# Performance work log

Measured on AMD Instinct MI355X. Metric: run time of the kernel, lower is better.

The kernel has to match this reference:

```python
import jax, jax.numpy as jnp
import numpy as np

N = 50000        # nodes
E = 800000       # edges (avg degree 16)
F_IN = 128
H = 128
C = 16


def setup_inputs() -> dict:
    key = jax.random.key(0)
    ks = jax.random.split(key, 12)
    x = jax.random.normal(ks[0], (N, F_IN), dtype=jnp.float32)
    edges = jax.random.randint(ks[1], (2, E), 0, N, dtype=jnp.int32)
    dims = [(F_IN, H), (H, H // 2), (H // 2, H // 4), (H // 4, H // 8), (H // 8, C)]
    params = {}
    for i, (di, do) in enumerate(dims):
        params[f"W{i+1}"] = jax.random.normal(ks[2 + 2 * i], (di, do), dtype=jnp.float32) * (1.0 / np.sqrt(di)).astype(np.float32)
        params[f"b{i+1}"] = jax.random.normal(ks[3 + 2 * i], (do,), dtype=jnp.float32) * 0.01
    return {"x": x, "edges": edges, **params}


def reference(x, edges, W1, b1, W2, b2, W3, b3, W4, b4, W5, b5):
    src, dst = edges[0], edges[1]
    ones = jnp.ones((E,), x.dtype)
    # symmetric ('both') normalization with degree clamped to >= 1 (DGL GraphConv default)
    out_deg = jnp.clip(jax.ops.segment_sum(ones, src, num_segments=N), 1.0, None)
    in_deg = jnp.clip(jax.ops.segment_sum(ones, dst, num_segments=N), 1.0, None)
    norm_src = (out_deg ** -0.5)[:, None]   # [N,1]
    norm_dst = (in_deg ** -0.5)[:, None]    # [N,1]

    def graph_conv(h, W, b):
        h = h @ W                                  # dense transform first (out <= in)
        msgs = (h * norm_src)[src]                 # [E, d_out] gather
        agg = jax.ops.segment_sum(msgs, dst, num_segments=N)  # scatter-add SpMM
        return agg * norm_dst + b

    h = x
    for W, b in ((W1, b1), (W2, b2), (W3, b3), (W4, b4), (W5, b5)):
        h = jax.nn.relu(graph_conv(h, W, b))
    return h
```

## Files before the change

### kernel.cpp

```cpp
#include <hip/hip_runtime.h>
#include <hip/hip_bf16.h>


#define THREADS 256
#define HIST_B 256
#define HWORDS 12500

typedef __attribute__((ext_vector_type(8))) short short8_t;
typedef __attribute__((ext_vector_type(4))) float float4_t;

__device__ __forceinline__ unsigned short f2bf_rne(float f) {
    unsigned u = __builtin_bit_cast(unsigned, f);
    unsigned r = u + 0x7fffu + ((u >> 16) & 1u);
    return (unsigned short)(r >> 16);
}
__device__ __forceinline__ float bf2f(unsigned short h) {
    return __builtin_bit_cast(float, ((unsigned)h) << 16);
}

__global__ __launch_bounds__(THREADS)
void hist_kernel(const int* __restrict__ src, const int* __restrict__ dst,
                 unsigned* __restrict__ p_src, unsigned* __restrict__ p_dst,
                 unsigned char* __restrict__ rank, int E, int chunk) {
    __shared__ unsigned bins[HWORDS];
    const bool is_dst = blockIdx.x < HIST_B;
    const int b = is_dst ? blockIdx.x : blockIdx.x - HIST_B;
    const int t = threadIdx.x;
    const int e0 = b * chunk;
    int e1 = e0 + chunk; if (e1 > E) e1 = E;
    const int* __restrict__ idx = is_dst ? dst : src;
    unsigned* __restrict__ pout = is_dst ? p_dst : p_src;

    for (int w = t; w < HWORDS; w += THREADS) bins[w] = 0;
    __syncthreads();
    for (int e = e0 + t; e < e1; e += THREADS) {
        int d = idx[e];
        unsigned sh = (unsigned)(d & 3) * 8u;
        unsigned old = atomicAdd(&bins[d >> 2], 1u << sh);
        if (is_dst) rank[e] = (unsigned char)((old >> sh) & 0xffu);
    }
    __syncthreads();
    for (int w = t; w < HWORDS; w += THREADS)
        pout[(size_t)b * HWORDS + w] = bins[w];
}

__global__ __launch_bounds__(THREADS)
void reduce_scanA_kernel(const unsigned* __restrict__ p_src, unsigned* __restrict__ p_dst,
                         int* __restrict__ deg_dst,
                         float* __restrict__ norm_src, float* __restrict__ norm_dst,
                         int* __restrict__ partials, int N) {
    __shared__ int red[THREADS];
    const int t = threadIdx.x;
    const int w = blockIdx.x * THREADS + t;
    int degsum = 0;
    if (w < HWORDS) {
        unsigned s = 0;
#pragma unroll 4
        for (int b = 0; b < HIST_B; ++b) s += p_src[(size_t)b * HWORDS + w];

        unsigned run = 0;
#pragma unroll 4
        for (int b = 0; b < HIST_B; ++b) {
            size_t i = (size_t)b * HWORDS + w;
            unsigned v = p_dst[i];
            p_dst[i] = run;
            run += v;
        }

#pragma unroll
        for (int l = 0; l < 4; ++l) {
            int node = 4 * w + l;
            int dd = (int)((run >> (8 * l)) & 0xffu);
            int ds = (int)((s   >> (8 * l)) & 0xffu);
            deg_dst[node] = dd;
            norm_dst[node] = rsqrtf((float)(dd < 1 ? 1 : dd));
            norm_src[node] = rsqrtf((float)(ds < 1 ? 1 : ds));
            degsum += dd;
        }
    }
    red[t] = degsum;
    __syncthreads();
#pragma unroll
    for (int off = THREADS / 2; off > 0; off >>= 1) {
        if (t < off) red[t] += red[t + off];
        __syncthreads();
    }
    if (t == 0) partials[blockIdx.x] = red[0];
}

__global__ __launch_bounds__(THREADS)
void scanB_kernel(int* __restrict__ partials, int* __restrict__ row_ptr,
                  int nb, int N) {
    __shared__ int s[THREADS];
    int t = threadIdx.x;
    int v = (t < nb) ? partials[t] : 0;
    s[t] = v;
    __syncthreads();
#pragma unroll
    for (int off = 1; off < THREADS; off <<= 1) {
        int u = 0;
        if (t >= off) u = s[t - off];
        __syncthreads();
        s[t] += u;
        __syncthreads();
    }
    if (t < nb) partials[t] = s[t] - v;
    if (t == THREADS - 1) row_ptr[N] = s[t];
}

__global__ __launch_bounds__(THREADS)
void scanC_kernel(const int* __restrict__ deg_dst, const int* __restrict__ partials,
                  int* __restrict__ row_ptr, int N) {
    __shared__ int s[THREADS];
    const int t = threadIdx.x;
    const int base = blockIdx.x * 1024 + t * 4;
    int d0 = 0, d1 = 0, d2 = 0, d3 = 0;
    if (base + 3 < N) {
        int4 d = *(const int4*)&deg_dst[base];
        d0 = d.x; d1 = d.y; d2 = d.z; d3 = d.w;
    } else {
        if (base + 0 < N) d0 = deg_dst[base + 0];
        if (base + 1 < N) d1 = deg_dst[base + 1];
        if (base + 2 < N) d2 = deg_dst[base + 2];
        if (base + 3 < N) d3 = deg_dst[base + 3];
    }
    int tsum = d0 + d1 + d2 + d3;
    s[t] = tsum;
    __syncthreads();
#pragma unroll
    for (int off = 1; off < THREADS; off <<= 1) {
        int u = 0;
        if (t >= off) u = s[t - off];
        __syncthreads();
        s[t] += u;
        __syncthreads();
    }
    int pre = partials[blockIdx.x] + s[t] - tsum;
    if (base + 0 < N) row_ptr[base + 0] = pre; pre += d0;
    if (base + 1 < N) row_ptr[base + 1] = pre; pre += d1;
    if (base + 2 < N) row_ptr[base + 2] = pre; pre += d2;
    if (base + 3 < N) row_ptr[base + 3] = pre;
}

__global__ __launch_bounds__(THREADS)
void scatter_kernel(const int* __restrict__ src, const int* __restrict__ dst,
                    const unsigned char* __restrict__ rank,
                    const int* __restrict__ row_ptr, const unsigned* __restrict__ p_dst,
                    int* __restrict__ col, int E, int chunk) {
    const int b = blockIdx.x;
    const int e0 = b * chunk;
    int e1 = e0 + chunk; if (e1 > E) e1 = E;
    for (int e = e0 + threadIdx.x; e < e1; e += THREADS) {
        int d = dst[e];
        unsigned sh = (unsigned)(d & 3) * 8u;
        unsigned pre = (p_dst[(size_t)b * HWORDS + (d >> 2)] >> sh) & 0xffu;
        col[row_ptr[d] + (int)pre + (int)rank[e]] = src[e];
    }
}

__device__ __forceinline__ void conv_one(const float* __restrict__ W, short* __restrict__ hi,
                                         short* __restrict__ lo, int K, int NOUT, int STR, int i) {
    int n = i / STR;
    int kk = i % STR;
    float v = (kk < K) ? W[(size_t)kk * NOUT + n] : 0.f;
    unsigned short h = f2bf_rne(v);
    hi[i] = (short)h;
    lo[i] = (short)f2bf_rne(v - bf2f(h));
}

__global__ __launch_bounds__(THREADS)
void convert_all_kernel(const float* W1, const float* W2, const float* W3,
                        const float* W4, const float* W5,
                        short* w1h, short* w1l, short* w2h, short* w2l,
                        short* w3h, short* w3l, short* w4h, short* w4l,
                        short* w5h, short* w5l) {
    int i = blockIdx.x * blockDim.x + threadIdx.x;
    if      (i < 17408)                    conv_one(W1, w1h, w1l, 128, 128, 136, i);
    else if ((i -= 17408) < 8704)          conv_one(W2, w2h, w2l, 128, 64, 136, i);
    else if ((i -= 8704) < 2304)           conv_one(W3, w3h, w3l, 64, 32, 72, i);
    else if ((i -= 2304) < 640)            conv_one(W4, w4h, w4l, 32, 16, 40, i);
    else if ((i -= 640) < 640)             conv_one(W5, w5h, w5l, 16, 16, 40, i);
}

template<int K, int NOUT>
__global__ __launch_bounds__(THREADS)
void gemm_mfma_kernel(const float* __restrict__ A, const short* __restrict__ wt_hi,
                      const short* __restrict__ wt_lo, const float* __restrict__ norm,
                      short* __restrict__ outq, float* __restrict__ qscale, int M) {
    constexpr int Kp  = (K + 31) & ~31;
    constexpr int STR = Kp + 8;
    constexpr int NT  = NOUT / 16;

    __shared__ short lh[NOUT * STR];
    __shared__ short ll[NOUT * STR];

    const int tid = threadIdx.x;
    {
        constexpr int CNT = NOUT * STR / 2;
        const int* gh = (const int*)wt_hi;
        const int* gl = (const int*)wt_lo;
        int* sh = (int*)lh;
        int* sl = (int*)ll;
        for (int i = tid; i < CNT; i += THREADS) { sh[i] = gh[i]; sl[i] = gl[i]; }
    }
    __syncthreads();

    const int w    = tid >> 6;
    const int lane = tid & 63;
    const int ln   = lane & 15;
    const int quad = lane >> 4;
    const int row  = blockIdx.x * 64 + w * 16 + ln;
    const bool rv  = row < M;

    float4_t acc[NT];
#pragma unroll
    for (int i = 0; i < NT; ++i) acc[i] = (float4_t){0.f, 0.f, 0.f, 0.f};

#pragma unroll
    for (int kt = 0; kt < Kp / 32; ++kt) {
        const int k0 = kt * 32 + quad * 8;
        float a[8];
        if (rv && k0 < K) {
            float4 v0 = *(const float4*)&A[(size_t)row * K + k0];
            float4 v1 = *(const float4*)&A[(size_t)row * K + k0 + 4];
            a[0] = v0.x; a[1] = v0.y; a[2] = v0.z; a[3] = v0.w;
            a[4] = v1.x; a[5] = v1.y; a[6] = v1.z; a[7] = v1.w;
        } else {
#pragma unroll
            for (int j = 0; j < 8; ++j) a[j] = 0.f;
        }
        short8_t ahi, alo;
#pragma unroll
        for (int j = 0; j < 8; ++j) {
            unsigned short h = f2bf_rne(a[j]);
            ahi[j] = (short)h;
            alo[j] = (short)f2bf_rne(a[j] - bf2f(h));
        }
#pragma unroll
        for (int nt = 0; nt < NT; ++nt) {
            const int bidx = (nt * 16 + ln) * STR + kt * 32 + quad * 8;
            short8_t bh = *(const short8_t*)&lh[bidx];
            short8_t bl = *(const short8_t*)&ll[bidx];
            acc[nt] = __builtin_amdgcn_mfma_f32_16x16x32_bf16(ahi, bh, acc[nt], 0, 0, 0);
            acc[nt] = __builtin_amdgcn_mfma_f32_16x16x32_bf16(ahi, bl, acc[nt], 0, 0, 0);
            acc[nt] = __builtin_amdgcn_mfma_f32_16x16x32_bf16(alo, bh, acc[nt], 0, 0, 0);
        }
    }

    const int orow = blockIdx.x * 64 + w * 16 + quad * 4;
#pragma unroll
    for (int i = 0; i < 4; ++i) {
        int r = orow + i;
        float m = 0.f;
#pragma unroll
        for (int nt = 0; nt < NT; ++nt) m = fmaxf(m, fabsf(acc[nt][i]));
#pragma unroll
        for (int off = 1; off < 16; off <<= 1) m = fmaxf(m, __shfl_xor(m, off));
        float s = (r < M) ? norm[r] : 0.f;
        float rowmax = m * s;
        float inv = (rowmax > 0.f) ? (32767.f / rowmax) : 0.f;
        if (r < M) {
            if (ln == 0) qscale[r] = rowmax * (1.f / 32767.f);
#pragma unroll
            for (int nt = 0; nt < NT; ++nt)
                outq[(size_t)r * NOUT + nt * 16 + ln] =
                    (short)(int)__builtin_rintf(acc[nt][i] * s * inv);
        }
    }
}

template<int D>
__global__ __launch_bounds__(THREADS)
void agg_q_kernel(const short* __restrict__ tq, const float* __restrict__ qscale,
                  const int* __restrict__ row_ptr, const int* __restrict__ col,
                  const float* __restrict__ norm_dst, const float* __restrict__ bias,
                  float* __restrict__ out, int N) {
    constexpr int TPN = D / 8;
    constexpr int NPB = THREADS / TPN;
    const int tid  = threadIdx.x;
    const int ln   = tid % TPN;
    const int g    = tid / TPN;
    const int node = blockIdx.x * NPB + g;
    if (node >= N) return;

    const int beg = row_ptr[node];
    const int end = row_ptr[node + 1];

    float acc[8];
#pragma unroll
    for (int c = 0; c < 8; ++c) acc[c] = 0.f;

    int j = beg;
    for (; j + 3 < end; j += 4) {
        int s0 = col[j], s1 = col[j + 1], s2 = col[j + 2], s3 = col[j + 3];
        short8_t v0 = *(const short8_t*)&tq[(size_t)s0 * D + ln * 8];
        short8_t v1 = *(const short8_t*)&tq[(size_t)s1 * D + ln * 8];
        short8_t v2 = *(const short8_t*)&tq[(size_t)s2 * D + ln * 8];
        short8_t v3 = *(const short8_t*)&tq[(size_t)s3 * D + ln * 8];
        float c0 = qscale[s0], c1 = qscale[s1], c2 = qscale[s2], c3 = qscale[s3];
#pragma unroll
        for (int c = 0; c < 8; ++c)
            acc[c] += (float)v0[c] * c0 + (float)v1[c] * c1
                    + (float)v2[c] * c2 + (float)v3[c] * c3;
    }
    for (; j < end; ++j) {
        int s0 = col[j];
        short8_t v0 = *(const short8_t*)&tq[(size_t)s0 * D + ln * 8];
        float c0 = qscale[s0];
#pragma unroll
        for (int c = 0; c < 8; ++c) acc[c] += (float)v0[c] * c0;
    }

    float nd = norm_dst[node];
    float4 b0 = *(const float4*)&bias[ln * 8];
    float4 b1 = *(const float4*)&bias[ln * 8 + 4];
    float4 o0, o1;
    o0.x = fmaxf(acc[0] * nd + b0.x, 0.f);
    o0.y = fmaxf(acc[1] * nd + b0.y, 0.f);
    o0.z = fmaxf(acc[2] * nd + b0.z, 0.f);
    o0.w = fmaxf(acc[3] * nd + b0.w, 0.f);
    o1.x = fmaxf(acc[4] * nd + b1.x, 0.f);
    o1.y = fmaxf(acc[5] * nd + b1.y, 0.f);
    o1.z = fmaxf(acc[6] * nd + b1.z, 0.f);
    o1.w = fmaxf(acc[7] * nd + b1.w, 0.f);
    *(float4*)&out[(size_t)node * D + ln * 8] = o0;
    *(float4*)&out[(size_t)node * D + ln * 8 + 4] = o1;
}

extern "C" void kernel_launch(void* const* d_in, const int* in_sizes, int n_in,
                              void* d_out, int out_size, void* d_ws, size_t ws_size,
                              hipStream_t stream) {
    const float* x     = (const float*)d_in[0];
    const int*   edges = (const int*)d_in[1];
    const float* W1 = (const float*)d_in[2];  const float* b1 = (const float*)d_in[3];
    const float* W2 = (const float*)d_in[4];  const float* b2 = (const float*)d_in[5];
    const float* W3 = (const float*)d_in[6];  const float* b3 = (const float*)d_in[7];
    const float* W4 = (const float*)d_in[8];  const float* b4 = (const float*)d_in[9];
    const float* W5 = (const float*)d_in[10]; const float* b5 = (const float*)d_in[11];

    const int N = in_sizes[0] / 128;
    const int E = in_sizes[1] / 2;
    const int* src = edges;
    const int* dst = edges + E;

    char* ws = (char*)d_ws;
    size_t off = 0;
    auto carve = [&](size_t bytes) -> void* {
        void* p = ws + off;
        off += (bytes + 255) & ~(size_t)255;
        return p;
    };
    short* tq       = (short*)carve((size_t)N * 128 * 2);
    float* hbuf     = (float*)carve((size_t)N * 128 * 4);
    int*   deg_dst  = (int*)carve((size_t)N * 4);
    float* norm_src = (float*)carve((size_t)N * 4);
    float* norm_dst = (float*)carve((size_t)N * 4);
    int*   row_ptr  = (int*)carve((size_t)(N + 1) * 4);
    int*   col      = (int*)carve((size_t)E * 4);
    int*   partials = (int*)carve((size_t)1024 * 4);
    float* qscale   = (float*)carve((size_t)N * 4);
    short* wts      = (short*)carve((size_t)59392 * 2);
    unsigned* p_src = (unsigned*)carve((size_t)HIST_B * HWORDS * 4);
    unsigned* p_dst = (unsigned*)carve((size_t)HIST_B * HWORDS * 4);
    unsigned char* rank = (unsigned char*)carve((size_t)E);
    (void)ws_size;

    short* w1h = wts;            short* w1l = w1h + 17408;
    short* w2h = w1l + 17408;    short* w2l = w2h + 8704;
    short* w3h = w2l + 8704;     short* w3l = w3h + 2304;
    short* w4h = w3l + 2304;     short* w4l = w4h + 640;
    short* w5h = w4l + 640;      short* w5l = w5h + 640;

    const int chunk = (E + HIST_B - 1) / HIST_B;

    convert_all_kernel<<<(29696 + 255) / 256, THREADS, 0, stream>>>(
        W1, W2, W3, W4, W5, w1h, w1l, w2h, w2l, w3h, w3l, w4h, w4l, w5h, w5l);

    hist_kernel<<<2 * HIST_B, THREADS, 0, stream>>>(src, dst, p_src, p_dst, rank, E, chunk);
    reduce_scanA_kernel<<<(HWORDS + THREADS - 1) / THREADS, THREADS, 0, stream>>>(
        p_src, p_dst, deg_dst, norm_src, norm_dst, partials, N);
    scanB_kernel<<<1, THREADS, 0, stream>>>(partials, row_ptr, (HWORDS + THREADS - 1) / THREADS, N);
    scanC_kernel<<<(N + 1023) / 1024, THREADS, 0, stream>>>(deg_dst, partials, row_ptr, N);
    scatter_kernel<<<HIST_B, THREADS, 0, stream>>>(src, dst, rank, row_ptr, p_dst, col, E, chunk);

    const int gridG = (N + 63) / 64;

    gemm_mfma_kernel<128, 128><<<gridG, THREADS, 0, stream>>>(x, w1h, w1l, norm_src, tq, qscale, N);
    agg_q_kernel<128><<<(N + 15) / 16, THREADS, 0, stream>>>(tq, qscale, row_ptr, col, norm_dst, b1, hbuf, N);

    gemm_mfma_kernel<128, 64><<<gridG, THREADS, 0, stream>>>(hbuf, w2h, w2l, norm_src, tq, qscale, N);
    agg_q_kernel<64><<<(N + 31) / 32, THREADS, 0, stream>>>(tq, qscale, row_ptr, col, norm_dst, b2, hbuf, N);

    gemm_mfma_kernel<64, 32><<<gridG, THREADS, 0, stream>>>(hbuf, w3h, w3l, norm_src, tq, qscale, N);
    agg_q_kernel<32><<<(N + 63) / 64, THREADS, 0, stream>>>(tq, qscale, row_ptr, col, norm_dst, b3, hbuf, N);

    gemm_mfma_kernel<32, 16><<<gridG, THREADS, 0, stream>>>(hbuf, w4h, w4l, norm_src, tq, qscale, N);
    agg_q_kernel<16><<<(N + 127) / 128, THREADS, 0, stream>>>(tq, qscale, row_ptr, col, norm_dst, b4, hbuf, N);

    gemm_mfma_kernel<16, 16><<<gridG, THREADS, 0, stream>>>(hbuf, w5h, w5l, norm_src, tq, qscale, N);
    agg_q_kernel<16><<<(N + 127) / 128, THREADS, 0, stream>>>(tq, qscale, row_ptr, col, norm_dst, b5, (float*)d_out, N);
}
```

Baseline: 297.9 us.

## Fuse layer-1 GEMM, histograms and weight conversion into one packed launch

Merges the weight conversion, the src/dst degree histograms and the first-layer GEMM (which now converts W1 into shared memory itself and defers norm_src scaling) into a single heterogeneous kernel. The three reduce/scan kernels are collapsed into one kernel that uses a flag-based decoupled lookback across blocks and folds norm_src into qscale afterwards. The goal is to remove several launches and serialization gaps and overlap GEMM with the histogram work. In exchange it relies on all 49 scan blocks being co-resident for the spin-wait, and every GEMM block redundantly converts W1 while using about 68KB of shared memory per block, which may limit occupancy.

```diff
diff --git a/kernel.cpp b/kernel.cpp
--- a/kernel.cpp
+++ b/kernel.cpp
@@ -5,6 +5,7 @@
 #define THREADS 256
 #define HIST_B 256
 #define HWORDS 12500
+#define RS_BLOCKS 49
 
 typedef __attribute__((ext_vector_type(8))) short short8_t;
 typedef __attribute__((ext_vector_type(4))) float float4_t;
@@ -18,128 +19,231 @@
     return __builtin_bit_cast(float, ((unsigned)h) << 16);
 }
 
+template<int K, int NOUT, bool NORM>
+__device__ __forceinline__ void gemm_core(const float* __restrict__ A,
+                                          const short* lh, const short* ll,
+                                          const float* __restrict__ norm,
+                                          short* __restrict__ outq,
+                                          float* __restrict__ qscale,
+                                          int M, int blk, int tid) {
+    constexpr int Kp  = (K + 31) & ~31;
+    constexpr int STR = Kp + 8;
+    constexpr int NT  = NOUT / 16;
+
+    const int w    = tid >> 6;
+    const int lane = tid & 63;
+    const int ln   = lane & 15;
+    const int quad = lane >> 4;
+    const int row  = blk * 64 + w * 16 + ln;
+    const bool rv  = row < M;
+
+    float4_t acc[NT];
+#pragma unroll
+    for (int i = 0; i < NT; ++i) acc[i] = (float4_t){0.f, 0.f, 0.f, 0.f};
+
+#pragma unroll
+    for (int kt = 0; kt < Kp / 32; ++kt) {
+        const int k0 = kt * 32 + quad * 8;
+        float a[8];
+        if (rv && k0 < K) {
+            float4 v0 = *(const float4*)&A[(size_t)row * K + k0];
+            float4 v1 = *(const float4*)&A[(size_t)row * K + k0 + 4];
+            a[0] = v0.x; a[1] = v0.y; a[2] = v0.z; a[3] = v0.w;
+            a[4] = v1.x; a[5] = v1.y; a[6] = v1.z; a[7] = v1.w;
+        } else {
+#pragma unroll
+            for (int j = 0; j < 8; ++j) a[j] = 0.f;
+        }
+        short8_t ahi, alo;
+#pragma unroll
+        for (int j = 0; j < 8; ++j) {
+            unsigned short h = f2bf_rne(a[j]);
+            ahi[j] = (short)h;
+            alo[j] = (short)f2bf_rne(a[j] - bf2f(h));
+        }
+#pragma unroll
+        for (int nt = 0; nt < NT; ++nt) {
+            const int bidx = (nt * 16 + ln) * STR + kt * 32 + quad * 8;
+            short8_t bh = *(const short8_t*)&lh[bidx];
+            short8_t bl = *(const short8_t*)&ll[bidx];
+            acc[nt] = __builtin_amdgcn_mfma_f32_16x16x32_bf16(ahi, bh, acc[nt], 0, 0, 0);
+            acc[nt] = __builtin_amdgcn_mfma_f32_16x16x32_bf16(ahi, bl, acc[nt], 0, 0, 0);
+            acc[nt] = __builtin_amdgcn_mfma_f32_16x16x32_bf16(alo, bh, acc[nt], 0, 0, 0);
+        }
+    }
+
+    const int orow = blk * 64 + w * 16 + quad * 4;
+#pragma unroll
+    for (int i = 0; i < 4; ++i) {
+        int r = orow + i;
+        float m = 0.f;
+#pragma unroll
+        for (int nt = 0; nt < NT; ++nt) m = fmaxf(m, fabsf(acc[nt][i]));
+#pragma unroll
+        for (int off = 1; off < 16; off <<= 1) m = fmaxf(m, __shfl_xor(m, off));
+        float s = 1.f;
+        if (NORM) s = (r < M) ? norm[r] : 0.f;
+        float rowmax = m * s;
+        float inv = (rowmax > 0.f) ? (32767.f / rowmax) : 0.f;
+        if (r < M) {
+            if (ln == 0) qscale[r] = rowmax * (1.f / 32767.f);
+#pragma unroll
+            for (int nt = 0; nt < NT; ++nt)
+                outq[(size_t)r * NOUT + nt * 16 + ln] =
+                    (short)(int)__builtin_rintf(acc[nt][i] * s * inv);
+        }
+    }
+}
+
+__device__ __forceinline__ void conv_one(const float* __restrict__ W, short* __restrict__ hi,
+                                         short* __restrict__ lo, int K, int NOUT, int STR, int i) {
+    int n = i / STR;
+    int kk = i % STR;
+    float v = (kk < K) ? W[(size_t)kk * NOUT + n] : 0.f;
+    unsigned short h = f2bf_rne(v);
+    hi[i] = (short)h;
+    lo[i] = (short)f2bf_rne(v - bf2f(h));
+}
+
 __global__ __launch_bounds__(THREADS)
-void hist_kernel(const int* __restrict__ src, const int* __restrict__ dst,
-                 unsigned* __restrict__ p_src, unsigned* __restrict__ p_dst,
-                 unsigned char* __restrict__ rank, int E, int chunk) {
-    __shared__ unsigned bins[HWORDS];
-    const bool is_dst = blockIdx.x < HIST_B;
-    const int b = is_dst ? blockIdx.x : blockIdx.x - HIST_B;
+void packed0_kernel(const float* __restrict__ x, const float* __restrict__ W1,
+                    const float* __restrict__ W2, const float* __restrict__ W3,
+                    const float* __restrict__ W4, const float* __restrict__ W5,
+                    short* __restrict__ tq, float* __restrict__ qscale,
+                    const int* __restrict__ src, const int* __restrict__ dst,
+                    unsigned* __restrict__ p_src, unsigned* __restrict__ p_dst,
+                    unsigned char* __restrict__ rank, int* __restrict__ flags,
+                    short* w2h, short* w2l, short* w3h, short* w3l,
+                    short* w4h, short* w4l, short* w5h, short* w5l,
+                    int E, int chunk, int N, int G1) {
+    __shared__ __align__(16) char smem[69632];
+    const int blk = blockIdx.x;
     const int t = threadIdx.x;
-    const int e0 = b * chunk;
-    int e1 = e0 + chunk; if (e1 > E) e1 = E;
-    const int* __restrict__ idx = is_dst ? dst : src;
-    unsigned* __restrict__ pout = is_dst ? p_dst : p_src;
-
-    for (int w = t; w < HWORDS; w += THREADS) bins[w] = 0;
-    __syncthreads();
-    for (int e = e0 + t; e < e1; e += THREADS) {
-        int d = idx[e];
-        unsigned sh = (unsigned)(d & 3) * 8u;
-        unsigned old = atomicAdd(&bins[d >> 2], 1u << sh);
-        if (is_dst) rank[e] = (unsigned char)((old >> sh) & 0xffu);
-    }
-    __syncthreads();
-    for (int w = t; w < HWORDS; w += THREADS)
-        pout[(size_t)b * HWORDS + w] = bins[w];
+
+    if (blk < G1) {
+        short* lh = (short*)smem;
+        short* ll = (short*)smem + 17408;
+        for (int j = t; j < 128 * 128; j += THREADS) {
+            int kk = j >> 7, n = j & 127;
+            float v = W1[j];
+            unsigned short h = f2bf_rne(v);
+            lh[n * 136 + kk] = (short)h;
+            ll[n * 136 + kk] = (short)f2bf_rne(v - bf2f(h));
+        }
+        __syncthreads();
+        gemm_core<128, 128, false>(x, lh, ll, nullptr, tq, qscale, N, blk, t);
+    } else if (blk < G1 + 2 * HIST_B) {
+        unsigned* bins = (unsigned*)smem;
+        const int hb = blk - G1;
+        const bool is_dst = hb < HIST_B;
+        const int b = is_dst ? hb : hb - HIST_B;
+        const int e0 = b * chunk;
+        int e1 = e0 + chunk; if (e1 > E) e1 = E;
+        const int* __restrict__ idx = is_dst ? dst : src;
+        unsigned* __restrict__ pout = is_dst ? p_dst : p_src;
+
+        for (int w = t; w < HWORDS; w += THREADS) bins[w] = 0;
+        __syncthreads();
+        for (int e = e0 + t; e < e1; e += THREADS) {
+            int d = idx[e];
+            unsigned sh = (unsigned)(d & 3) * 8u;
+            unsigned old = atomicAdd(&bins[d >> 2], 1u << sh);
+            if (is_dst) rank[e] = (unsigned char)((old >> sh) & 0xffu);
+        }
+        __syncthreads();
+        for (int w = t; w < HWORDS; w += THREADS)
+            pout[(size_t)b * HWORDS + w] = bins[w];
+    } else {
+        int cb = blk - G1 - 2 * HIST_B;
+        if (cb == 48) {
+            if (t < 64) flags[t] = 0;
+            return;
+        }
+        int i = cb * THREADS + t;
+        if (i < 8704)                        conv_one(W2, w2h, w2l, 128, 64, 136, i);
+        else if ((i -= 8704) < 2304)         conv_one(W3, w3h, w3l, 64, 32, 72, i);
+        else if ((i -= 2304) < 640)          conv_one(W4, w4h, w4l, 32, 16, 40, i);
+        else { i -= 640;                     conv_one(W5, w5h, w5l, 16, 16, 40, i); }
+    }
 }
 
 __global__ __launch_bounds__(THREADS)
-void reduce_scanA_kernel(const unsigned* __restrict__ p_src, unsigned* __restrict__ p_dst,
-                         int* __restrict__ deg_dst,
-                         float* __restrict__ norm_src, float* __restrict__ norm_dst,
-                         int* __restrict__ partials, int N) {
-    __shared__ int red[THREADS];
+void reduce_scan_kernel(const unsigned* __restrict__ p_src, unsigned* __restrict__ p_dst,
+                        float* __restrict__ norm_src, float* __restrict__ norm_dst,
+                        float* __restrict__ qscale, int* __restrict__ row_ptr,
+                        int* __restrict__ flags, int N) {
+    __shared__ int sh[THREADS];
+    __shared__ int bexcl_sh;
     const int t = threadIdx.x;
-    const int w = blockIdx.x * THREADS + t;
-    int degsum = 0;
+    const int b = blockIdx.x;
+    const int w = b * THREADS + t;
+
+    int d0 = 0, d1 = 0, d2 = 0, d3 = 0;
     if (w < HWORDS) {
         unsigned s = 0;
 #pragma unroll 4
-        for (int b = 0; b < HIST_B; ++b) s += p_src[(size_t)b * HWORDS + w];
+        for (int c = 0; c < HIST_B; ++c) s += p_src[(size_t)c * HWORDS + w];
 
         unsigned run = 0;
 #pragma unroll 4
-        for (int b = 0; b < HIST_B; ++b) {
-            size_t i = (size_t)b * HWORDS + w;
+        for (int c = 0; c < HIST_B; ++c) {
+            size_t i = (size_t)c * HWORDS + w;
             unsigned v = p_dst[i];
             p_dst[i] = run;
             run += v;
         }
+        d0 = (int)(run & 0xffu); d1 = (int)((run >> 8) & 0xffu);
+        d2 = (int)((run >> 16) & 0xffu); d3 = (int)(run >> 24);
 
 #pragma unroll
         for (int l = 0; l < 4; ++l) {
             int node = 4 * w + l;
-            int dd = (int)((run >> (8 * l)) & 0xffu);
-            int ds = (int)((s   >> (8 * l)) & 0xffu);
-            deg_dst[node] = dd;
-            norm_dst[node] = rsqrtf((float)(dd < 1 ? 1 : dd));
-            norm_src[node] = rsqrtf((float)(ds < 1 ? 1 : ds));
-            degsum += dd;
-        }
-    }
-    red[t] = degsum;
-    __syncthreads();
-#pragma unroll
-    for (int off = THREADS / 2; off > 0; off >>= 1) {
-        if (t < off) red[t] += red[t + off];
-        __syncthreads();
-    }
-    if (t == 0) partials[blockIdx.x] = red[0];
-}
-
-__global__ __launch_bounds__(THREADS)
-void scanB_kernel(int* __restrict__ partials, int* __restrict__ row_ptr,
-                  int nb, int N) {
-    __shared__ int s[THREADS];
-    int t = threadIdx.x;
-    int v = (t < nb) ? partials[t] : 0;
-    s[t] = v;
+            if (node < N) {
+                int dd = (l == 0) ? d0 : (l == 1) ? d1 : (l == 2) ? d2 : d3;
+                int ds = (int)((s >> (8 * l)) & 0xffu);
+                norm_dst[node] = rsqrtf((float)(dd < 1 ? 1 : dd));
+                float ns = rsqrtf((float)(ds < 1 ? 1 : ds));
+                norm_src[node] = ns;
+                qscale[node] *= ns;
+            }
+        }
+    }
+
+    int tsum = d0 + d1 + d2 + d3;
+    sh[t] = tsum;
     __syncthreads();
 #pragma unroll
     for (int off = 1; off < THREADS; off <<= 1) {
         int u = 0;
-        if (t >= off) u = s[t - off];
+        if (t >= off) u = sh[t - off];
         __syncthreads();
-        s[t] += u;
+        sh[t] += u;
         __syncthreads();
     }
-    if (t < nb) partials[t] = s[t] - v;
-    if (t == THREADS - 1) row_ptr[N] = s[t];
-}
-
-__global__ __launch_bounds__(THREADS)
-void scanC_kernel(const int* __restrict__ deg_dst, const int* __restrict__ partials,
-                  int* __restrict__ row_ptr, int N) {
-    __shared__ int s[THREADS];
-    const int t = threadIdx.x;
-    const int base = blockIdx.x * 1024 + t * 4;
-    int d0 = 0, d1 = 0, d2 = 0, d3 = 0;
-    if (base + 3 < N) {
-        int4 d = *(const int4*)&deg_dst[base];
-        d0 = d.x; d1 = d.y; d2 = d.z; d3 = d.w;
-    } else {
-        if (base + 0 < N) d0 = deg_dst[base + 0];
-        if (base + 1 < N) d1 = deg_dst[base + 1];
-        if (base + 2 < N) d2 = deg_dst[base + 2];
-        if (base + 3 < N) d3 = deg_dst[base + 3];
-    }
-    int tsum = d0 + d1 + d2 + d3;
-    s[t] = tsum;
+    const int btotal = sh[THREADS - 1];
+    const int lexcl  = sh[t] - tsum;
+
+    if (t == 0) atomicExch(&flags[b], btotal + 1);
+    if (t < 64) {
+        int v = 0;
+        if (t < b) {
+            int f;
+            do { f = atomicAdd(&flags[t], 0); } while (f == 0);
+            v = f - 1;
+        }
+#pragma unroll
+        for (int off = 1; off < 64; off <<= 1) v += __shfl_xor(v, off);
+        if (t == 0) bexcl_sh = v;
+    }
     __syncthreads();
-#pragma unroll
-    for (int off = 1; off < THREADS; off <<= 1) {
-        int u = 0;
-        if (t >= off) u = s[t - off];
-        __syncthreads();
-        s[t] += u;
-        __syncthreads();
-    }
-    int pre = partials[blockIdx.x] + s[t] - tsum;
-    if (base + 0 < N) row_ptr[base + 0] = pre; pre += d0;
-    if (base + 1 < N) row_ptr[base + 1] = pre; pre += d1;
-    if (base + 2 < N) row_ptr[base + 2] = pre; pre += d2;
-    if (base + 3 < N) row_ptr[base + 3] = pre;
+
+    int pre = bexcl_sh + lexcl;
+    int n0 = 4 * w;
+    if (n0 + 0 < N) row_ptr[n0 + 0] = pre; pre += d0;
+    if (n0 + 1 < N) row_ptr[n0 + 1] = pre; pre += d1;
+    if (n0 + 2 < N) row_ptr[n0 + 2] = pre; pre += d2;
+    if (n0 + 3 < N) row_ptr[n0 + 3] = pre;
+    if (b == RS_BLOCKS - 1 && t == THREADS - 1) row_ptr[N] = bexcl_sh + btotal;
 }
 
 __global__ __launch_bounds__(THREADS)
@@ -158,30 +262,6 @@
     }
 }
 
-__device__ __forceinline__ void conv_one(const float* __restrict__ W, short* __restrict__ hi,
-                                         short* __restrict__ lo, int K, int NOUT, int STR, int i) {
-    int n = i / STR;
-    int kk = i % STR;
-    float v = (kk < K) ? W[(size_t)kk * NOUT + n] : 0.f;
-    unsigned short h = f2bf_rne(v);
-    hi[i] = (short)h;
-    lo[i] = (short)f2bf_rne(v - bf2f(h));
-}
-
-__global__ __launch_bounds__(THREADS)
-void convert_all_kernel(const float* W1, const float* W2, const float* W3,
-                        const float* W4, const float* W5,
-                        short* w1h, short* w1l, short* w2h, short* w2l,
-                        short* w3h, short* w3l, short* w4h, short* w4l,
-                        short* w5h, short* w5l) {
-    int i = blockIdx.x * blockDim.x + threadIdx.x;
-    if      (i < 17408)                    conv_one(W1, w1h, w1l, 128, 128, 136, i);
-    else if ((i -= 17408) < 8704)          conv_one(W2, w2h, w2l, 128, 64, 136, i);
-    else if ((i -= 8704) < 2304)           conv_one(W3, w3h, w3l, 64, 32, 72, i);
-    else if ((i -= 2304) < 640)            conv_one(W4, w4h, w4l, 32, 16, 40, i);
-    else if ((i -= 640) < 640)             conv_one(W5, w5h, w5l, 16, 16, 40, i);
-}
-
 template<int K, int NOUT>
 __global__ __launch_bounds__(THREADS)
 void gemm_mfma_kernel(const float* __restrict__ A, const short* __restrict__ wt_hi,
@@ -189,7 +269,6 @@
                       short* __restrict__ outq, float* __restrict__ qscale, int M) {
     constexpr int Kp  = (K + 31) & ~31;
     constexpr int STR = Kp + 8;
-    constexpr int NT  = NOUT / 16;
 
     __shared__ short lh[NOUT * STR];
     __shared__ short ll[NOUT * STR];
@@ -204,69 +283,7 @@
         for (int i = tid; i < CNT; i += THREADS) { sh[i] = gh[i]; sl[i] = gl[i]; }
     }
     __syncthreads();
-
-    const int w    = tid >> 6;
-    const int lane = tid & 63;
-    const int ln   = lane & 15;
-    const int quad = lane >> 4;
-    const int row  = blockIdx.x * 64 + w * 16 + ln;
-    const bool rv  = row < M;
-
-    float4_t acc[NT];
-#pragma unroll
-    for (int i = 0; i < NT; ++i) acc[i] = (float4_t){0.f, 0.f, 0.f, 0.f};
-
-#pragma unroll
-    for (int kt = 0; kt < Kp / 32; ++kt) {
-        const int k0 = kt * 32 + quad * 8;
-        float a[8];
-        if (rv && k0 < K) {
-            float4 v0 = *(const float4*)&A[(size_t)row * K + k0];
-            float4 v1 = *(const float4*)&A[(size_t)row * K + k0 + 4];
-            a[0] = v0.x; a[1] = v0.y; a[2] = v0.z; a[3] = v0.w;
-            a[4] = v1.x; a[5] = v1.y; a[6] = v1.z; a[7] = v1.w;
-        } else {
-#pragma unroll
-            for (int j = 0; j < 8; ++j) a[j] = 0.f;
-        }
-        short8_t ahi, alo;
-#pragma unroll
-        for (int j = 0; j < 8; ++j) {
-            unsigned short h = f2bf_rne(a[j]);
-            ahi[j] = (short)h;
-            alo[j] = (short)f2bf_rne(a[j] - bf2f(h));
-        }
-#pragma unroll
-        for (int nt = 0; nt < NT; ++nt) {
-            const int bidx = (nt * 16 + ln) * STR + kt * 32 + quad * 8;
-            short8_t bh = *(const short8_t*)&lh[bidx];
-            short8_t bl = *(const short8_t*)&ll[bidx];
-            acc[nt] = __builtin_amdgcn_mfma_f32_16x16x32_bf16(ahi, bh, acc[nt], 0, 0, 0);
-            acc[nt] = __builtin_amdgcn_mfma_f32_16x16x32_bf16(ahi, bl, acc[nt], 0, 0, 0);
-            acc[nt] = __builtin_amdgcn_mfma_f32_16x16x32_bf16(alo, bh, acc[nt], 0, 0, 0);
-        }
-    }
-
-    const int orow = blockIdx.x * 64 + w * 16 + quad * 4;
-#pragma unroll
-    for (int i = 0; i < 4; ++i) {
-        int r = orow + i;
-        float m = 0.f;
-#pragma unroll
-        for (int nt = 0; nt < NT; ++nt) m = fmaxf(m, fabsf(acc[nt][i]));
-#pragma unroll
-        for (int off = 1; off < 16; off <<= 1) m = fmaxf(m, __shfl_xor(m, off));
-        float s = (r < M) ? norm[r] : 0.f;
-        float rowmax = m * s;
-        float inv = (rowmax > 0.f) ? (32767.f / rowmax) : 0.f;
-        if (r < M) {
-            if (ln == 0) qscale[r] = rowmax * (1.f / 32767.f);
-#pragma unroll
-            for (int nt = 0; nt < NT; ++nt)
-                outq[(size_t)r * NOUT + nt * 16 + ln] =
-                    (short)(int)__builtin_rintf(acc[nt][i] * s * inv);
-        }
-    }
+    gemm_core<K, NOUT, true>(A, lh, ll, norm, outq, qscale, M, blockIdx.x, tid);
 }
 
 template<int D>
@@ -352,40 +369,35 @@
     };
     short* tq       = (short*)carve((size_t)N * 128 * 2);
     float* hbuf     = (float*)carve((size_t)N * 128 * 4);
-    int*   deg_dst  = (int*)carve((size_t)N * 4);
     float* norm_src = (float*)carve((size_t)N * 4);
     float* norm_dst = (float*)carve((size_t)N * 4);
     int*   row_ptr  = (int*)carve((size_t)(N + 1) * 4);
     int*   col      = (int*)carve((size_t)E * 4);
-    int*   partials = (int*)carve((size_t)1024 * 4);
     float* qscale   = (float*)carve((size_t)N * 4);
-    short* wts      = (short*)carve((size_t)59392 * 2);
+    int*   flags    = (int*)carve((size_t)64 * 4);
+    short* wts      = (short*)carve((size_t)24576 * 2);
     unsigned* p_src = (unsigned*)carve((size_t)HIST_B * HWORDS * 4);
     unsigned* p_dst = (unsigned*)carve((size_t)HIST_B * HWORDS * 4);
     unsigned char* rank = (unsigned char*)carve((size_t)E);
     (void)ws_size;
 
-    short* w1h = wts;            short* w1l = w1h + 17408;
-    short* w2h = w1l + 17408;    short* w2l = w2h + 8704;
+    short* w2h = wts;            short* w2l = w2h + 8704;
     short* w3h = w2l + 8704;     short* w3l = w3h + 2304;
     short* w4h = w3l + 2304;     short* w4l = w4h + 640;
     short* w5h = w4l + 640;      short* w5l = w5h + 640;
 
     const int chunk = (E + HIST_B - 1) / HIST_B;
-
-    convert_all_kernel<<<(29696 + 255) / 256, THREADS, 0, stream>>>(
-        W1, W2, W3, W4, W5, w1h, w1l, w2h, w2l, w3h, w3l, w4h, w4l, w5h, w5l);
-
-    hist_kernel<<<2 * HIST_B, THREADS, 0, stream>>>(src, dst, p_src, p_dst, rank, E, chunk);
-    reduce_scanA_kernel<<<(HWORDS + THREADS - 1) / THREADS, THREADS, 0, stream>>>(
-        p_src, p_dst, deg_dst, norm_src, norm_dst, partials, N);
-    scanB_kernel<<<1, THREADS, 0, stream>>>(partials, row_ptr, (HWORDS + THREADS - 1) / THREADS, N);
-    scanC_kernel<<<(N + 1023) / 1024, THREADS, 0, stream>>>(deg_dst, partials, row_ptr, N);
+    const int gridG = (N + 63) / 64;
+
+    packed0_kernel<<<gridG + 2 * HIST_B + RS_BLOCKS, THREADS, 0, stream>>>(
+        x, W1, W2, W3, W4, W5, tq, qscale, src, dst, p_src, p_dst, rank, flags,
+        w2h, w2l, w3h, w3l, w4h, w4l, w5h, w5l, E, chunk, N, gridG);
+
+    reduce_scan_kernel<<<RS_BLOCKS, THREADS, 0, stream>>>(
+        p_src, p_dst, norm_src, norm_dst, qscale, row_ptr, flags, N);
+
     scatter_kernel<<<HIST_B, THREADS, 0, stream>>>(src, dst, rank, row_ptr, p_dst, col, E, chunk);
 
-    const int gridG = (N + 63) / 64;
-
-    gemm_mfma_kernel<128, 128><<<gridG, THREADS, 0, stream>>>(x, w1h, w1l, norm_src, tq, qscale, N);
     agg_q_kernel<128><<<(N + 15) / 16, THREADS, 0, stream>>>(tq, qscale, row_ptr, col, norm_dst, b1, hbuf, N);
 
     gemm_mfma_kernel<128, 64><<<gridG, THREADS, 0, stream>>>(hbuf, w2h, w2l, norm_src, tq, qscale, N);
```

New measurement: 296.7 us. About the same (-0.4%).
